# Kernel optimization log

Hardware: AMD Instinct MI355X
Metric: run time of the kernel (lower is better)

Reference implementation:

```python
import jax, jax.numpy as jnp
import numpy as np

N_ATOMS = 8192
N_FINGERPRINT = 10000
DIM = 64
N_LAYERS = 3
N_MOL = 256


def setup_inputs() -> dict:
    key = jax.random.key(0)
    k1, k2, k3, k4, k5 = jax.random.split(key, 5)
    fingerprints = jax.random.randint(k1, (N_ATOMS,), 0, N_FINGERPRINT)
    adjacencies = jax.random.uniform(k2, (N_ATOMS, N_ATOMS), dtype=jnp.float32)
    segment_ids = jnp.sort(jax.random.randint(k3, (N_ATOMS,), 0, N_MOL))
    embed_table = jax.random.normal(k4, (N_FINGERPRINT, DIM), dtype=jnp.float32) * 0.1
    W = jax.random.normal(k5, (N_LAYERS, DIM, DIM), dtype=jnp.float32) * (1.0 / np.sqrt(DIM))
    b = jnp.zeros((N_LAYERS, DIM), dtype=jnp.float32)
    return {"fingerprints": fingerprints, "adjacencies": adjacencies,
            "segment_ids": segment_ids, "embed_table": embed_table, "W": W, "b": b}


def reference(fingerprints, adjacencies, segment_ids, embed_table, W, b):
    # Embed fingerprint indices -> [N_atoms, dim]
    vectors = embed_table[fingerprints]
    # MPNN layers: h = relu(Linear(v)); v = h + A @ h  (residual message passing)
    for layer in range(N_LAYERS):
        h = jax.nn.relu(jnp.einsum('nd,ed->ne', vectors, W[layer]) + b[layer])
        vectors = h + adjacencies @ h
    # Sum pooling per molecule (torch.split + sum == segment_sum over sorted ids)
    molecular_vectors = jax.ops.segment_sum(vectors, segment_ids, num_segments=N_MOL)
    return molecular_vectors
```

## Files before the change

kernel.cpp:

```cpp
#include <hip/hip_runtime.h>

#define N_ATOMS 8192
#define DIM 64
#define N_MOL 256
#define KS 16
#define KCH (N_ATOMS / KS)
#define BM 64
#define BN 64
#define BK 64
#define NSTEP (KCH / BK)

typedef __attribute__((ext_vector_type(8))) short short8v;
typedef __attribute__((ext_vector_type(4))) float f32x4;
typedef unsigned short ushort_t;

__device__ __forceinline__ ushort_t f2bf(float x) {
    unsigned u = __float_as_uint(x);
    u += 0x7fffu + ((u >> 16) & 1u);
    return (ushort_t)(u >> 16);
}

__device__ __forceinline__ void gload16(const void* gsrc, void* ldst) {
    __builtin_amdgcn_global_load_lds(
        (const __attribute__((address_space(1))) void*)gsrc,
        (__attribute__((address_space(3))) void*)ldst, 16, 0, 0);
}

__global__ __launch_bounds__(256) void convsa_kernel(
        const float* __restrict__ A, const int* __restrict__ seg,
        ushort_t* __restrict__ Abf, float* __restrict__ SAf32) {
    const int t = threadIdx.x;
    const int k = blockIdx.x * 512 + t * 2;
    const int n0 = blockIdx.y * 128;
    __shared__ int segs[128];
    if (t < 128) segs[t] = seg[n0 + t];
    __syncthreads();

    float a0 = 0.f, a1 = 0.f;
    int prev = segs[0];
    for (int ni = 0; ni < 128; ni += 4) {
        float2 v0 = *(const float2*)(A + (size_t)(n0 + ni + 0) * N_ATOMS + k);
        float2 v1 = *(const float2*)(A + (size_t)(n0 + ni + 1) * N_ATOMS + k);
        float2 v2 = *(const float2*)(A + (size_t)(n0 + ni + 2) * N_ATOMS + k);
        float2 v3 = *(const float2*)(A + (size_t)(n0 + ni + 3) * N_ATOMS + k);
        float2 vs[4] = {v0, v1, v2, v3};
#pragma unroll
        for (int j = 0; j < 4; ++j) {
            const int m = segs[ni + j];
            if (m != prev) {
                atomicAdd(&SAf32[(size_t)prev * N_ATOMS + k],     a0);
                atomicAdd(&SAf32[(size_t)prev * N_ATOMS + k + 1], a1);
                a0 = a1 = 0.f; prev = m;
            }
            ushort2 bv; bv.x = f2bf(vs[j].x); bv.y = f2bf(vs[j].y);
            *(ushort2*)(Abf + (size_t)(n0 + ni + j) * N_ATOMS + k) = bv;
            a0 += vs[j].x; a1 += vs[j].y;
        }
    }
    atomicAdd(&SAf32[(size_t)prev * N_ATOMS + k],     a0);
    atomicAdd(&SAf32[(size_t)prev * N_ATOMS + k + 1], a1);
}

__global__ __launch_bounds__(256) void packsa_kernel(
        const float* __restrict__ SAf32, ushort_t* __restrict__ SAbf) {
    const size_t i = ((size_t)blockIdx.x * 256 + threadIdx.x) * 8;
    float4 x0 = *(const float4*)(SAf32 + i);
    float4 x1 = *(const float4*)(SAf32 + i + 4);
    short8v v;
    v[0] = (short)f2bf(x0.x); v[1] = (short)f2bf(x0.y);
    v[2] = (short)f2bf(x0.z); v[3] = (short)f2bf(x0.w);
    v[4] = (short)f2bf(x1.x); v[5] = (short)f2bf(x1.y);
    v[6] = (short)f2bf(x1.z); v[7] = (short)f2bf(x1.w);
    *(short8v*)(SAbf + i) = v;
}

template <int FIRST, int LAST>
__global__ __launch_bounds__(256) void fused_linear_kernel(
        const int* __restrict__ fp, const float* __restrict__ table,
        const float* __restrict__ vprev, const int* __restrict__ seg,
        const float* __restrict__ W, const float* __restrict__ b,
        float* __restrict__ vnext, ushort_t* __restrict__ hT,
        float* __restrict__ out) {
    __shared__ float Ws[DIM][DIM + 1];
    __shared__ float vsT[DIM][36];
    __shared__ int segs[32];

    const int t = threadIdx.x;
    const int n0 = blockIdx.x * 32;
    if (LAST && t < 32) segs[t] = seg[n0 + t];
    for (int i = t; i < DIM * DIM; i += 256) Ws[i >> 6][i & 63] = W[i];
    for (int i = t; i < 32 * DIM; i += 256) {
        const int nl = i >> 6, d = i & 63;
        const size_t n = n0 + nl;
        float val;
        if (FIRST) val = table[(size_t)fp[n] * DIM + d];
        else       val = vprev[n * DIM + d];
        vsT[d][nl] = val;
    }
    __syncthreads();

    const int e = t & 63;
    const int g = t >> 6;
    float acc[8];
    const float be = b[e];
#pragma unroll
    for (int i = 0; i < 8; ++i) acc[i] = be;

    for (int d = 0; d < DIM; ++d) {
        const float w = Ws[e][d];
        const float4* vp = (const float4*)&vsT[d][g * 8];
        float4 x0 = vp[0], x1 = vp[1];
        acc[0] += w * x0.x; acc[1] += w * x0.y; acc[2] += w * x0.z; acc[3] += w * x0.w;
        acc[4] += w * x1.x; acc[5] += w * x1.y; acc[6] += w * x1.z; acc[7] += w * x1.w;
    }

    ushort_t hb[8];
    float seg_acc = 0.f;
    int prev = LAST ? segs[g * 8] : 0;
#pragma unroll
    for (int i = 0; i < 8; ++i) {
        float hv = acc[i] > 0.f ? acc[i] : 0.f;
        if (LAST) {
            const int m = segs[g * 8 + i];
            if (m != prev) {
                atomicAdd(&out[(size_t)prev * DIM + e], seg_acc);
                seg_acc = 0.f; prev = m;
            }
            seg_acc += hv;
        } else {
            vnext[(size_t)(n0 + g * 8 + i) * DIM + e] = hv;
        }
        hb[i] = f2bf(hv);
    }
    if (LAST) atomicAdd(&out[(size_t)prev * DIM + e], seg_acc);
    *(short8v*)(hT + (size_t)e * N_ATOMS + n0 + g * 8) = *(short8v*)&hb[0];
}

__global__ __launch_bounds__(256) void matmul_mfma_kernel(
        const ushort_t* __restrict__ Abf, const ushort_t* __restrict__ hT,
        float* __restrict__ vnext) {
    __shared__ ushort_t Asw[2][BM * BK];
    __shared__ ushort_t Bsw[2][BN * BK];

    const int t  = threadIdx.x;
    const int w  = t >> 6;
    const int l  = t & 63;
    const int lm = l & 15;
    const int lq = l >> 4;
    const int r0 = blockIdx.x * BM;
    const size_t kc0 = (size_t)blockIdx.y * KCH;

    auto stage = [&](int bi, size_t kb) {
#pragma unroll
        for (int q = 0; q < 2; ++q) {
            const int i = q * 256 + t;
            const int r = i >> 3, s = i & 7;
            gload16(Abf + (size_t)(r0 + r) * N_ATOMS + kb + ((s ^ (r & 7)) << 3),
                    &Asw[bi][(q * 256 + w * 64) * 8]);
        }
#pragma unroll
        for (int q = 0; q < 2; ++q) {
            const int i = q * 256 + t;
            const int r = i >> 3, s = i & 7;
            gload16(hT + (size_t)r * N_ATOMS + kb + ((s ^ (r & 7)) << 3),
                    &Bsw[bi][(q * 256 + w * 64) * 8]);
        }
    };

    f32x4 acc[4];
#pragma unroll
    for (int n = 0; n < 4; ++n) acc[n] = (f32x4){0.f, 0.f, 0.f, 0.f};

    stage(0, kc0);

    for (int ks = 0; ks < NSTEP; ++ks) {
        const int bi = ks & 1;
        if (ks + 1 < NSTEP) {
            stage(bi ^ 1, kc0 + (size_t)(ks + 1) * BK);
            asm volatile("s_waitcnt vmcnt(4)" ::: "memory");
        } else {
            asm volatile("s_waitcnt vmcnt(0)" ::: "memory");
        }
        __builtin_amdgcn_s_barrier();
        asm volatile("" ::: "memory");
#pragma unroll
        for (int kki = 0; kki < 2; ++kki) {
            const int sx = ((kki * 4 + lq) ^ (lm & 7)) << 3;
            const int ra = w * 16 + lm;
            short8v a0 = *(const short8v*)&Asw[bi][ra * BK + sx];
            short8v b0 = *(const short8v*)&Bsw[bi][(lm)      * BK + sx];
            short8v b1 = *(const short8v*)&Bsw[bi][(lm + 16) * BK + sx];
            short8v b2 = *(const short8v*)&Bsw[bi][(lm + 32) * BK + sx];
            short8v b3 = *(const short8v*)&Bsw[bi][(lm + 48) * BK + sx];
            acc[0] = __builtin_amdgcn_mfma_f32_16x16x32_bf16(a0, b0, acc[0], 0, 0, 0);
            acc[1] = __builtin_amdgcn_mfma_f32_16x16x32_bf16(a0, b1, acc[1], 0, 0, 0);
            acc[2] = __builtin_amdgcn_mfma_f32_16x16x32_bf16(a0, b2, acc[2], 0, 0, 0);
            acc[3] = __builtin_amdgcn_mfma_f32_16x16x32_bf16(a0, b3, acc[3], 0, 0, 0);
        }
        asm volatile("" ::: "memory");
        __builtin_amdgcn_s_barrier();
        asm volatile("" ::: "memory");
    }

    const int rb = r0 + w * 16 + lq * 4;
#pragma unroll
    for (int j = 0; j < 4; ++j) {
        float* vp = vnext + (size_t)(rb + j) * DIM + lm;
#pragma unroll
        for (int n = 0; n < 4; ++n) atomicAdd(vp + n * 16, acc[n][j]);
    }
}

extern "C" void kernel_launch(void* const* d_in, const int* in_sizes, int n_in,
                              void* d_out, int out_size, void* d_ws, size_t ws_size,
                              hipStream_t stream) {
    const int*   fp    = (const int*)d_in[0];
    const float* A     = (const float*)d_in[1];
    const int*   seg   = (const int*)d_in[2];
    const float* table = (const float*)d_in[3];
    const float* W     = (const float*)d_in[4];
    const float* b     = (const float*)d_in[5];
    float* out = (float*)d_out;

    char* ws = (char*)d_ws;
    float*    vA    = (float*)    ws;
    float*    vB    = (float*)   (ws + 2097152);
    ushort_t* hT    = (ushort_t*)(ws + 4194304);
    float*    SAf32 = (float*)   (ws + 5242880);
    ushort_t* SAbf  = (ushort_t*)(ws + 13631488);
    ushort_t* Abf   = (ushort_t*)(ws + 17825792);

    (void)hipMemsetAsync(SAf32, 0, (size_t)N_MOL * N_ATOMS * 4, stream);
    (void)hipMemsetAsync(out, 0, (size_t)out_size * 4, stream);

    convsa_kernel<<<dim3(16, 64), 256, 0, stream>>>(A, seg, Abf, SAf32);
    packsa_kernel<<<(N_MOL * N_ATOMS) / (256 * 8), 256, 0, stream>>>(SAf32, SAbf);

    dim3 mmgrid(N_ATOMS / BM, KS);

    fused_linear_kernel<1, 0><<<N_ATOMS / 32, 256, 0, stream>>>(
        fp, table, nullptr, seg, W, b, vA, hT, nullptr);
    matmul_mfma_kernel<<<mmgrid, 256, 0, stream>>>(Abf, hT, vA);
    fused_linear_kernel<0, 0><<<N_ATOMS / 32, 256, 0, stream>>>(
        fp, table, vA, seg, W + DIM * DIM, b + DIM, vB, hT, nullptr);
    matmul_mfma_kernel<<<mmgrid, 256, 0, stream>>>(Abf, hT, vB);
    fused_linear_kernel<0, 1><<<N_ATOMS / 32, 256, 0, stream>>>(
        fp, table, vB, seg, W + 2 * DIM * DIM, b + 2 * DIM, nullptr, hT, out);
    matmul_mfma_kernel<<<dim3(N_MOL / BM, KS), 256, 0, stream>>>(SAbf, hT, out);
}
```

Before: 218.7 us.

## Fuse fp32-to-bf16 adjacency conversion and segment pre-reduction into first matmul

```diff
diff --git a/kernel.cpp b/kernel.cpp
--- a/kernel.cpp
+++ b/kernel.cpp
@@ -19,46 +19,14 @@
     u += 0x7fffu + ((u >> 16) & 1u);
     return (ushort_t)(u >> 16);
 }
+__device__ __forceinline__ float bf2f(ushort_t u) {
+    return __uint_as_float(((unsigned)u) << 16);
+}
 
 __device__ __forceinline__ void gload16(const void* gsrc, void* ldst) {
     __builtin_amdgcn_global_load_lds(
         (const __attribute__((address_space(1))) void*)gsrc,
         (__attribute__((address_space(3))) void*)ldst, 16, 0, 0);
-}
-
-__global__ __launch_bounds__(256) void convsa_kernel(
-        const float* __restrict__ A, const int* __restrict__ seg,
-        ushort_t* __restrict__ Abf, float* __restrict__ SAf32) {
-    const int t = threadIdx.x;
-    const int k = blockIdx.x * 512 + t * 2;
-    const int n0 = blockIdx.y * 128;
-    __shared__ int segs[128];
-    if (t < 128) segs[t] = seg[n0 + t];
-    __syncthreads();
-
-    float a0 = 0.f, a1 = 0.f;
-    int prev = segs[0];
-    for (int ni = 0; ni < 128; ni += 4) {
-        float2 v0 = *(const float2*)(A + (size_t)(n0 + ni + 0) * N_ATOMS + k);
-        float2 v1 = *(const float2*)(A + (size_t)(n0 + ni + 1) * N_ATOMS + k);
-        float2 v2 = *(const float2*)(A + (size_t)(n0 + ni + 2) * N_ATOMS + k);
-        float2 v3 = *(const float2*)(A + (size_t)(n0 + ni + 3) * N_ATOMS + k);
-        float2 vs[4] = {v0, v1, v2, v3};
-#pragma unroll
-        for (int j = 0; j < 4; ++j) {
-            const int m = segs[ni + j];
-            if (m != prev) {
-                atomicAdd(&SAf32[(size_t)prev * N_ATOMS + k],     a0);
-                atomicAdd(&SAf32[(size_t)prev * N_ATOMS + k + 1], a1);
-                a0 = a1 = 0.f; prev = m;
-            }
-            ushort2 bv; bv.x = f2bf(vs[j].x); bv.y = f2bf(vs[j].y);
-            *(ushort2*)(Abf + (size_t)(n0 + ni + j) * N_ATOMS + k) = bv;
-            a0 += vs[j].x; a1 += vs[j].y;
-        }
-    }
-    atomicAdd(&SAf32[(size_t)prev * N_ATOMS + k],     a0);
-    atomicAdd(&SAf32[(size_t)prev * N_ATOMS + k + 1], a1);
 }
 
 __global__ __launch_bounds__(256) void packsa_kernel(
@@ -136,11 +104,13 @@
     *(short8v*)(hT + (size_t)e * N_ATOMS + n0 + g * 8) = *(short8v*)&hb[0];
 }
 
-__global__ __launch_bounds__(256) void matmul_mfma_kernel(
-        const ushort_t* __restrict__ Abf, const ushort_t* __restrict__ hT,
-        float* __restrict__ vnext) {
+__global__ __launch_bounds__(256) void matmul_cvtsa_kernel(
+        const float* __restrict__ A, const int* __restrict__ seg,
+        ushort_t* __restrict__ Abf, float* __restrict__ SAf32,
+        const ushort_t* __restrict__ hT, float* __restrict__ vnext) {
     __shared__ ushort_t Asw[2][BM * BK];
     __shared__ ushort_t Bsw[2][BN * BK];
+    __shared__ int segs[BM];
 
     const int t  = threadIdx.x;
     const int w  = t >> 6;
@@ -150,13 +120,23 @@
     const int r0 = blockIdx.x * BM;
     const size_t kc0 = (size_t)blockIdx.y * KCH;
 
+    if (t < BM) segs[t] = seg[r0 + t];
+
     auto stage = [&](int bi, size_t kb) {
 #pragma unroll
         for (int q = 0; q < 2; ++q) {
             const int i = q * 256 + t;
             const int r = i >> 3, s = i & 7;
-            gload16(Abf + (size_t)(r0 + r) * N_ATOMS + kb + ((s ^ (r & 7)) << 3),
-                    &Asw[bi][(q * 256 + w * 64) * 8]);
+            const size_t goff = (size_t)(r0 + r) * N_ATOMS + kb + s * 8;
+            const float4* g = (const float4*)(A + goff);
+            float4 a0 = g[0], a1 = g[1];
+            short8v vv;
+            vv[0] = (short)f2bf(a0.x); vv[1] = (short)f2bf(a0.y);
+            vv[2] = (short)f2bf(a0.z); vv[3] = (short)f2bf(a0.w);
+            vv[4] = (short)f2bf(a1.x); vv[5] = (short)f2bf(a1.y);
+            vv[6] = (short)f2bf(a1.z); vv[7] = (short)f2bf(a1.w);
+            *(short8v*)&Asw[bi][r * BK + ((s ^ (r & 7)) << 3)] = vv;
+            *(short8v*)(Abf + goff) = vv;
         }
 #pragma unroll
         for (int q = 0; q < 2; ++q) {
@@ -177,9 +157,9 @@
         const int bi = ks & 1;
         if (ks + 1 < NSTEP) {
             stage(bi ^ 1, kc0 + (size_t)(ks + 1) * BK);
-            asm volatile("s_waitcnt vmcnt(4)" ::: "memory");
+            asm volatile("s_waitcnt vmcnt(2) lgkmcnt(0)" ::: "memory");
         } else {
-            asm volatile("s_waitcnt vmcnt(0)" ::: "memory");
+            asm volatile("s_waitcnt vmcnt(0) lgkmcnt(0)" ::: "memory");
         }
         __builtin_amdgcn_s_barrier();
         asm volatile("" ::: "memory");
@@ -197,6 +177,99 @@
             acc[2] = __builtin_amdgcn_mfma_f32_16x16x32_bf16(a0, b2, acc[2], 0, 0, 0);
             acc[3] = __builtin_amdgcn_mfma_f32_16x16x32_bf16(a0, b3, acc[3], 0, 0, 0);
         }
+        {
+            const int c  = t & 63;
+            const int cs = c >> 3, cj = c & 7;
+            const int kglob = (int)kc0 + ks * BK + c;
+            float sacc = 0.f;
+            int prev = segs[w * 16];
+#pragma unroll
+            for (int rr = 0; rr < 16; ++rr) {
+                const int row = w * 16 + rr;
+                const int m = segs[row];
+                if (m != prev) {
+                    atomicAdd(&SAf32[(size_t)prev * N_ATOMS + kglob], sacc);
+                    sacc = 0.f; prev = m;
+                }
+                sacc += bf2f(Asw[bi][row * BK + ((cs ^ (row & 7)) << 3) + cj]);
+            }
+            atomicAdd(&SAf32[(size_t)prev * N_ATOMS + kglob], sacc);
+        }
+        asm volatile("" ::: "memory");
+        __builtin_amdgcn_s_barrier();
+        asm volatile("" ::: "memory");
+    }
+
+    const int rb = r0 + w * 16 + lq * 4;
+#pragma unroll
+    for (int j = 0; j < 4; ++j) {
+        float* vp = vnext + (size_t)(rb + j) * DIM + lm;
+#pragma unroll
+        for (int n = 0; n < 4; ++n) atomicAdd(vp + n * 16, acc[n][j]);
+    }
+}
+
+__global__ __launch_bounds__(256) void matmul_mfma_kernel(
+        const ushort_t* __restrict__ Abf, const ushort_t* __restrict__ hT,
+        float* __restrict__ vnext) {
+    __shared__ ushort_t Asw[2][BM * BK];
+    __shared__ ushort_t Bsw[2][BN * BK];
+
+    const int t  = threadIdx.x;
+    const int w  = t >> 6;
+    const int l  = t & 63;
+    const int lm = l & 15;
+    const int lq = l >> 4;
+    const int r0 = blockIdx.x * BM;
+    const size_t kc0 = (size_t)blockIdx.y * KCH;
+
+    auto stage = [&](int bi, size_t kb) {
+#pragma unroll
+        for (int q = 0; q < 2; ++q) {
+            const int i = q * 256 + t;
+            const int r = i >> 3, s = i & 7;
+            gload16(Abf + (size_t)(r0 + r) * N_ATOMS + kb + ((s ^ (r & 7)) << 3),
+                    &Asw[bi][(q * 256 + w * 64) * 8]);
+        }
+#pragma unroll
+        for (int q = 0; q < 2; ++q) {
+            const int i = q * 256 + t;
+            const int r = i >> 3, s = i & 7;
+            gload16(hT + (size_t)r * N_ATOMS + kb + ((s ^ (r & 7)) << 3),
+                    &Bsw[bi][(q * 256 + w * 64) * 8]);
+        }
+    };
+
+    f32x4 acc[4];
+#pragma unroll
+    for (int n = 0; n < 4; ++n) acc[n] = (f32x4){0.f, 0.f, 0.f, 0.f};
+
+    stage(0, kc0);
+
+    for (int ks = 0; ks < NSTEP; ++ks) {
+        const int bi = ks & 1;
+        if (ks + 1 < NSTEP) {
+            stage(bi ^ 1, kc0 + (size_t)(ks + 1) * BK);
+            asm volatile("s_waitcnt vmcnt(4)" ::: "memory");
+        } else {
+            asm volatile("s_waitcnt vmcnt(0)" ::: "memory");
+        }
+        __builtin_amdgcn_s_barrier();
+        asm volatile("" ::: "memory");
+#pragma unroll
+        for (int kki = 0; kki < 2; ++kki) {
+            const int sx = ((kki * 4 + lq) ^ (lm & 7)) << 3;
+            const int ra = w * 16 + lm;
+            short8v a0 = *(const short8v*)&Asw[bi][ra * BK + sx];
+            short8v b0 = *(const short8v*)&Bsw[bi][(lm)      * BK + sx];
+            short8v b1 = *(const short8v*)&Bsw[bi][(lm + 16) * BK + sx];
+            short8v b2 = *(const short8v*)&Bsw[bi][(lm + 32) * BK + sx];
+            short8v b3 = *(const short8v*)&Bsw[bi][(lm + 48) * BK + sx];
+            acc[0] = __builtin_amdgcn_mfma_f32_16x16x32_bf16(a0, b0, acc[0], 0, 0, 0);
+            acc[1] = __builtin_amdgcn_mfma_f32_16x16x32_bf16(a0, b1, acc[1], 0, 0, 0);
+            acc[2] = __builtin_amdgcn_mfma_f32_16x16x32_bf16(a0, b2, acc[2], 0, 0, 0);
+            acc[3] = __builtin_amdgcn_mfma_f32_16x16x32_bf16(a0, b3, acc[3], 0, 0, 0);
+        }
         asm volatile("" ::: "memory");
         __builtin_amdgcn_s_barrier();
         asm volatile("" ::: "memory");
@@ -233,14 +306,12 @@
     (void)hipMemsetAsync(SAf32, 0, (size_t)N_MOL * N_ATOMS * 4, stream);
     (void)hipMemsetAsync(out, 0, (size_t)out_size * 4, stream);
 
-    convsa_kernel<<<dim3(16, 64), 256, 0, stream>>>(A, seg, Abf, SAf32);
-    packsa_kernel<<<(N_MOL * N_ATOMS) / (256 * 8), 256, 0, stream>>>(SAf32, SAbf);
-
     dim3 mmgrid(N_ATOMS / BM, KS);
 
     fused_linear_kernel<1, 0><<<N_ATOMS / 32, 256, 0, stream>>>(
         fp, table, nullptr, seg, W, b, vA, hT, nullptr);
-    matmul_mfma_kernel<<<mmgrid, 256, 0, stream>>>(Abf, hT, vA);
+    matmul_cvtsa_kernel<<<mmgrid, 256, 0, stream>>>(A, seg, Abf, SAf32, hT, vA);
+    packsa_kernel<<<(N_MOL * N_ATOMS) / (256 * 8), 256, 0, stream>>>(SAf32, SAbf);
     fused_linear_kernel<0, 0><<<N_ATOMS / 32, 256, 0, stream>>>(
         fp, table, vA, seg, W + DIM * DIM, b + DIM, vB, hT, nullptr);
     matmul_mfma_kernel<<<mmgrid, 256, 0, stream>>>(Abf, hT, vB);
```

Measured after the change: 191.8 us. -12.3%, faster.
